# Kernel optimization log

Measured on AMD Instinct MI355X. Metric: run time of the kernel, lower is better.

Reference implementation:

```python
import jax, jax.numpy as jnp
import numpy as np

B, T, H = 64, 320, 256
D = 2 * H  # input_size; cat([cw, cell]) has dim 2*D which must equal 4*H


def setup_inputs() -> dict:
    key = jax.random.key(0)
    ks = jax.random.split(key, 10)
    sD = 1.0 / np.sqrt(D)
    sG = 1.0 / np.sqrt(2 * D)
    sH = 1.0 / np.sqrt(H)
    f32 = jnp.float32
    n = lambda k, shape, s: jax.random.normal(k, shape, dtype=f32) * s
    return {
        "v": n(ks[0], (B, T, D), 1.0),
        "W1": n(ks[1], (D, D), sD), "b1": jnp.zeros((D,), f32),
        "W2": n(ks[2], (D, D), sD), "b2": jnp.zeros((D,), f32),
        "Wg": n(ks[3], (2 * D, 2 * D), sG), "bg": jnp.zeros((2 * D,), f32),
        "Wih_f": n(ks[4], (3 * H, 2 * D), sG), "Whh_f": n(ks[5], (3 * H, H), sH),
        "bih_f": jnp.zeros((3 * H,), f32), "bhh_f": jnp.zeros((3 * H,), f32),
        "Wih_b": n(ks[6], (3 * H, 2 * D), sG), "Whh_b": n(ks[7], (3 * H, H), sH),
        "bih_b": jnp.zeros((3 * H,), f32), "bhh_b": jnp.zeros((3 * H,), f32),
    }


def _gru_cell(x, h, Wih, Whh, bih, bhh):
    # torch GRUCell math: gates ordered (r, z, n)
    gi = x @ Wih.T + bih          # (B, 3H)
    gh = h @ Whh.T + bhh          # (B, 3H)
    i_r, i_z, i_n = jnp.split(gi, 3, axis=-1)
    h_r, h_z, h_n = jnp.split(gh, 3, axis=-1)
    r = jax.nn.sigmoid(i_r + h_r)
    z = jax.nn.sigmoid(i_z + h_z)
    n = jnp.tanh(i_n + r * h_n)
    return (1.0 - z) * n + z * h


def reference(v, W1, b1, W2, b2, Wg, bg,
              Wih_f, Whh_f, bih_f, bhh_f,
              Wih_b, Whh_b, bih_b, bhh_b):
    # context_mult = linear2(v) is identical every timestep -> hoist out of loop
    cm = jnp.einsum('btd,ed->bte', v, W2) + b2          # (B, T, D)

    def step(carry, cw):
        hf, hb = carry                                   # (B, H) each
        cwm = cw @ W1.T + b1                             # (B, D)
        f = jnp.tanh(cwm[:, None, :] + cm)               # (B, T, D)
        scores = jnp.einsum('bd,btd->bt', cw, f)         # (B, T)
        attn = jax.nn.softmax(scores, axis=-1)
        cell = jnp.einsum('bt,btd->bd', attn, v)         # (B, D)
        pg = jnp.concatenate([cw, cell], axis=-1)        # (B, 2D) == (B, 4H)
        gate = jax.nn.sigmoid(pg @ Wg.T + bg)
        gi = pg * gate
        # length-1 bidirectional GRU step: each direction sees the same input
        hf2 = _gru_cell(gi, hf, Wih_f, Whh_f, bih_f, bhh_f)
        hb2 = _gru_cell(gi, hb, Wih_b, Whh_b, bih_b, bhh_b)
        return (hf2, hb2), jnp.concatenate([hf2, hb2], axis=-1)

    h0 = jnp.zeros((v.shape[0], H), v.dtype)
    _, hs = jax.lax.scan(step, (h0, h0), jnp.swapaxes(v, 0, 1))
    return hs  # (T, B, 2H)
```

## Files before the change

### kernel.cpp

```cpp
#include <hip/hip_runtime.h>

typedef unsigned short u16;
typedef __fp16 h2 __attribute__((ext_vector_type(2)));
typedef __attribute__((ext_vector_type(8))) short bf16x8;
typedef __attribute__((ext_vector_type(4))) float f32x4;

__device__ __forceinline__ float fast_exp(float x) { return __expf(x); }
__device__ __forceinline__ float fast_rcp(float x) { return __builtin_amdgcn_rcpf(x); }
__device__ __forceinline__ float fast_tanh(float x) {
  float e = fast_exp(2.0f * x);
  return 1.0f - 2.0f * fast_rcp(e + 1.0f);
}
__device__ __forceinline__ float fast_sigmoid(float x) {
  return fast_rcp(1.0f + fast_exp(-x));
}
__device__ __forceinline__ u16 f2bf(float x) {
  unsigned u = __float_as_uint(x);
  return (u16)((u + 0x7fffu + ((u >> 16) & 1u)) >> 16);
}
__device__ __forceinline__ float bf2f(u16 u) {
  return __uint_as_float(((unsigned)u) << 16);
}

__global__ __launch_bounds__(256)
void k_cvt(const float* __restrict__ src, u16* __restrict__ dst, int n4)
{
  int i = blockIdx.x * 256 + threadIdx.x;
  if (i < n4) {
    float4 x = ((const float4*)src)[i];
    ushort4 o;
    o.x = f2bf(x.x); o.y = f2bf(x.y); o.z = f2bf(x.z); o.w = f2bf(x.w);
    ((ushort4*)dst)[i] = o;
  }
}

__global__ __launch_bounds__(256)
void k_split(const float* __restrict__ src, u16* __restrict__ hi,
             u16* __restrict__ lo, int n4)
{
  int i = blockIdx.x * 256 + threadIdx.x;
  if (i < n4) {
    float4 x = ((const float4*)src)[i];
    ushort4 h, l;
    h.x = f2bf(x.x); l.x = f2bf(x.x - bf2f(h.x));
    h.y = f2bf(x.y); l.y = f2bf(x.y - bf2f(h.y));
    h.z = f2bf(x.z); l.z = f2bf(x.z - bf2f(h.z));
    h.w = f2bf(x.w); l.w = f2bf(x.w - bf2f(h.w));
    ((ushort4*)hi)[i] = h;
    ((ushort4*)lo)[i] = l;
  }
}

template<int EXPOUT>
__global__ __launch_bounds__(256)
void k_sgemm(const u16* __restrict__ Ahi, const u16* __restrict__ Alo,
             const u16* __restrict__ Whi, const u16* __restrict__ Wlo,
             const float* __restrict__ bias,
             float* __restrict__ C, int N, int K, int Tc, int t0)
{
  __shared__ alignas(16) u16 Ah[128][40];
  __shared__ alignas(16) u16 Al[128][40];
  __shared__ alignas(16) u16 Bh[128][40];
  __shared__ alignas(16) u16 Bl[128][40];
  const int tid = threadIdx.x;
  const int m0 = blockIdx.x * 128;
  const int n0 = blockIdx.y * 128;
  const int wave = tid >> 6, lane = tid & 63;
  const int wm = (wave & 1) * 64, wn = (wave >> 1) * 64;

  const u16 *pAh[2], *pAl[2], *pBh[2], *pBl[2];
#pragma unroll
  for (int r = 0; r < 2; ++r) {
    int row = r * 64 + (tid >> 2);
    int gm = m0 + row;
    int ar = (gm / Tc) * 320 + t0 + gm % Tc;
    pAh[r] = Ahi + (size_t)ar * K;
    pAl[r] = Alo + (size_t)ar * K;
    int gn = n0 + row;
    pBh[r] = Whi + (size_t)gn * K;
    pBl[r] = Wlo + (size_t)gn * K;
  }

  f32x4 acc[4][4];
#pragma unroll
  for (int a = 0; a < 4; ++a)
#pragma unroll
    for (int b = 0; b < 4; ++b) acc[a][b] = (f32x4){0.f, 0.f, 0.f, 0.f};

  const int lrow = lane & 15, lq = lane >> 4;

  for (int k0 = 0; k0 < K; k0 += 32) {
#pragma unroll
    for (int r = 0; r < 2; ++r) {
      int row = r * 64 + (tid >> 2);
      int kk = k0 + (tid & 3) * 8;
      *(int4*)&Ah[row][(tid & 3) * 8] = *(const int4*)(pAh[r] + kk);
      *(int4*)&Al[row][(tid & 3) * 8] = *(const int4*)(pAl[r] + kk);
      *(int4*)&Bh[row][(tid & 3) * 8] = *(const int4*)(pBh[r] + kk);
      *(int4*)&Bl[row][(tid & 3) * 8] = *(const int4*)(pBl[r] + kk);
    }
    __syncthreads();
    bf16x8 avh[4], avl[4], bvh[4], bvl[4];
#pragma unroll
    for (int f = 0; f < 4; ++f) {
      avh[f] = *(const bf16x8*)&Ah[wm + f * 16 + lrow][lq * 8];
      avl[f] = *(const bf16x8*)&Al[wm + f * 16 + lrow][lq * 8];
      bvh[f] = *(const bf16x8*)&Bh[wn + f * 16 + lrow][lq * 8];
      bvl[f] = *(const bf16x8*)&Bl[wn + f * 16 + lrow][lq * 8];
    }
#pragma unroll
    for (int mf = 0; mf < 4; ++mf)
#pragma unroll
      for (int nf = 0; nf < 4; ++nf) {
        acc[mf][nf] = __builtin_amdgcn_mfma_f32_16x16x32_bf16(
            avh[mf], bvh[nf], acc[mf][nf], 0, 0, 0);
        acc[mf][nf] = __builtin_amdgcn_mfma_f32_16x16x32_bf16(
            avh[mf], bvl[nf], acc[mf][nf], 0, 0, 0);
        acc[mf][nf] = __builtin_amdgcn_mfma_f32_16x16x32_bf16(
            avl[mf], bvh[nf], acc[mf][nf], 0, 0, 0);
      }
    __syncthreads();
  }

  const int c = lane & 15, rg = lane >> 4;
#pragma unroll
  for (int mf = 0; mf < 4; ++mf) {
#pragma unroll
    for (int r = 0; r < 4; ++r) {
      int m = m0 + wm + mf * 16 + rg * 4 + r;
#pragma unroll
      for (int nf = 0; nf < 4; ++nf) {
        int n = n0 + wn + nf * 16 + c;
        float x = acc[mf][nf][r] + bias[n];
        C[(size_t)m * N + n] = EXPOUT ? fast_exp(2.0f * x) : x;
      }
    }
  }
}

template<int MODE>
__global__ __launch_bounds__(256)
void k_mgemm(const u16* __restrict__ A1, int K1, int map1,
             const u16* __restrict__ A2,
             const u16* __restrict__ W16, const float* __restrict__ bias,
             const float* __restrict__ E1, const float* __restrict__ E2,
             void* __restrict__ Cout, int N, int K, int Tc, int t0)
{
  __shared__ alignas(16) u16 As[128][40];
  __shared__ alignas(16) u16 Bs[128][40];
  const int tid = threadIdx.x;
  const int m0 = blockIdx.x * 128;
  const int n0 = blockIdx.y * 128;
  const int wave = tid >> 6, lane = tid & 63;
  const int wm = (wave & 1) * 64, wn = (wave >> 1) * 64;
  const int K2 = K - K1;

  const u16* pA1r[2];
  const u16* pA2r[2];
  const u16* pWr[2];
#pragma unroll
  for (int r = 0; r < 2; ++r) {
    int row = r * 64 + (tid >> 2);
    int gm = m0 + row;
    int ar1 = map1 ? ((gm / Tc) * 320 + t0 + gm % Tc) : gm;
    pA1r[r] = A1 + (size_t)ar1 * K1;
    pA2r[r] = A2 ? (A2 + (size_t)gm * K2) : pA1r[r];
    pWr[r] = W16 + (size_t)(n0 + row) * K;
  }

  f32x4 acc[4][4];
#pragma unroll
  for (int a = 0; a < 4; ++a)
#pragma unroll
    for (int b = 0; b < 4; ++b) acc[a][b] = (f32x4){0.f, 0.f, 0.f, 0.f};

  const int lrow = lane & 15, lq = lane >> 4;

  for (int k0 = 0; k0 < K; k0 += 32) {
#pragma unroll
    for (int r = 0; r < 2; ++r) {
      int row = r * 64 + (tid >> 2);
      int kk = k0 + (tid & 3) * 8;
      const u16* s = (kk < K1) ? (pA1r[r] + kk) : (pA2r[r] + (kk - K1));
      *(int4*)&As[row][(tid & 3) * 8] = *(const int4*)s;
      *(int4*)&Bs[row][(tid & 3) * 8] = *(const int4*)(pWr[r] + kk);
    }
    __syncthreads();
    bf16x8 av[4], bv[4];
#pragma unroll
    for (int f = 0; f < 4; ++f) {
      av[f] = *(const bf16x8*)&As[wm + f * 16 + lrow][lq * 8];
      bv[f] = *(const bf16x8*)&Bs[wn + f * 16 + lrow][lq * 8];
    }
#pragma unroll
    for (int mf = 0; mf < 4; ++mf)
#pragma unroll
      for (int nf = 0; nf < 4; ++nf)
        acc[mf][nf] = __builtin_amdgcn_mfma_f32_16x16x32_bf16(
            av[mf], bv[nf], acc[mf][nf], 0, 0, 0);
    __syncthreads();
  }

  const int c = lane & 15, rg = lane >> 4;
#pragma unroll
  for (int mf = 0; mf < 4; ++mf) {
#pragma unroll
    for (int r = 0; r < 4; ++r) {
      int m = m0 + wm + mf * 16 + rg * 4 + r;
      int vrow = map1 ? ((m / Tc) * 320 + t0 + m % Tc) : m;
#pragma unroll
      for (int nf = 0; nf < 4; ++nf) {
        int n = n0 + wn + nf * 16 + c;
        float x = acc[mf][nf][r] + bias[n];
        if (MODE == 1) {
          float pg = (n < 512) ? E1[(size_t)vrow * 512 + n]
                               : E2[(size_t)m * 512 + (n - 512)];
          ((u16*)Cout)[(size_t)m * N + n] = f2bf(pg * fast_sigmoid(x));
        } else {
          ((float*)Cout)[(size_t)m * N + n] = x;
        }
      }
    }
  }
}

__global__ __launch_bounds__(256)
void k_scores(const float* __restrict__ v, const float* __restrict__ Ecwm,
              const float* __restrict__ Fcm, float* __restrict__ sc,
              int Tc, int t0)
{
  __shared__ float vs[32][68], fs[32][68], cs[32][68];
  const int b = blockIdx.x;
  const int tl0 = blockIdx.y * 32;
  const int s0 = blockIdx.z * 32;
  const int tid = threadIdx.x;
  const int tx = tid & 15, ty = tid >> 4;
  const float* srcV = v    + ((size_t)b * 320 + t0 + tl0) * 512;
  const float* srcF = Ecwm + ((size_t)b * Tc + tl0) * 512;
  const float* srcC = Fcm  + ((size_t)b * 320 + s0) * 512;
  float a00 = 0, a01 = 0, a10 = 0, a11 = 0;
  float vs0 = 0, vs1 = 0;
  for (int d0 = 0; d0 < 512; d0 += 64) {
#pragma unroll
    for (int r = 0; r < 2; ++r) {
      int f = r * 256 + tid;
      int row = f >> 4, qq = f & 15;
      *(float4*)&vs[row][qq * 4] = *(const float4*)(srcV + (size_t)row * 512 + d0 + qq * 4);
      *(float4*)&fs[row][qq * 4] = *(const float4*)(srcF + (size_t)row * 512 + d0 + qq * 4);
      *(float4*)&cs[row][qq * 4] = *(const float4*)(srcC + (size_t)row * 512 + d0 + qq * 4);
    }
    __syncthreads();
#pragma unroll 4
    for (int d = 0; d < 64; ++d) {
      float c0 = cs[tx][d], c1 = cs[tx + 16][d];
      float e0 = fs[ty][d], e1 = fs[ty + 16][d];
      float v0 = vs[ty][d], v1 = vs[ty + 16][d];
      vs0 += v0; vs1 += v1;
      a00 = fmaf(v0, fast_rcp(fmaf(e0, c0, 1.0f)), a00);
      a01 = fmaf(v0, fast_rcp(fmaf(e0, c1, 1.0f)), a01);
      a10 = fmaf(v1, fast_rcp(fmaf(e1, c0, 1.0f)), a10);
      a11 = fmaf(v1, fast_rcp(fmaf(e1, c1, 1.0f)), a11);
    }
    __syncthreads();
  }
  float* o = sc + (size_t)b * Tc * 320;
  o[(size_t)(tl0 + ty) * 320 + s0 + tx]           = vs0 - 2.0f * a00;
  o[(size_t)(tl0 + ty) * 320 + s0 + tx + 16]      = vs0 - 2.0f * a01;
  o[(size_t)(tl0 + ty + 16) * 320 + s0 + tx]      = vs1 - 2.0f * a10;
  o[(size_t)(tl0 + ty + 16) * 320 + s0 + tx + 16] = vs1 - 2.0f * a11;
}

__global__ __launch_bounds__(256)
void k_softmax(float* __restrict__ sc)
{
  int wave = threadIdx.x >> 6;
  int lane = threadIdx.x & 63;
  int row = blockIdx.x * 4 + wave;
  float* p = sc + (size_t)row * 320;
  float x[5];
  float mx = -1e30f;
#pragma unroll
  for (int j = 0; j < 5; ++j) { x[j] = p[lane + 64 * j]; mx = fmaxf(mx, x[j]); }
#pragma unroll
  for (int off = 32; off > 0; off >>= 1) mx = fmaxf(mx, __shfl_xor(mx, off));
  float s = 0.f;
#pragma unroll
  for (int j = 0; j < 5; ++j) { x[j] = fast_exp(x[j] - mx); s += x[j]; }
#pragma unroll
  for (int off = 32; off > 0; off >>= 1) s += __shfl_xor(s, off);
  float rinv = fast_rcp(s);
#pragma unroll
  for (int j = 0; j < 5; ++j) p[lane + 64 * j] = x[j] * rinv;
}

__global__ __launch_bounds__(256)
void k_cell(const float* __restrict__ attn, const float* __restrict__ v,
            float* __restrict__ cell, u16* __restrict__ cell16, int Tc)
{
  __shared__ float As[16][32], Bs[16][64];
  const int b = blockIdx.x;
  const int m0 = blockIdx.y * 32;
  const int n0 = blockIdx.z * 64;
  const int tid = threadIdx.x;
  const float* A = attn + (size_t)b * Tc * 320;
  const float* B = v + (size_t)b * 320 * 512;
  float acc[2][4];
#pragma unroll
  for (int i = 0; i < 2; ++i)
#pragma unroll
    for (int j = 0; j < 4; ++j) acc[i][j] = 0.f;
  const int tm = (tid & 15) * 2, tn = (tid >> 4) * 4;
  for (int k0 = 0; k0 < 320; k0 += 16) {
    if (tid < 128) {
      int row = tid >> 2, q = tid & 3;
      float4 x = *(const float4*)(A + (size_t)(m0 + row) * 320 + k0 + q * 4);
      As[q * 4 + 0][row] = x.x;
      As[q * 4 + 1][row] = x.y;
      As[q * 4 + 2][row] = x.z;
      As[q * 4 + 3][row] = x.w;
    }
    {
      int krow = tid >> 4, qq = tid & 15;
      *(float4*)&Bs[krow][qq * 4] =
          *(const float4*)(B + (size_t)(k0 + krow) * 512 + n0 + qq * 4);
    }
    __syncthreads();
#pragma unroll
    for (int k = 0; k < 16; ++k) {
      float a0 = As[k][tm], a1 = As[k][tm + 1];
      float bb[4];
      *(float4*)&bb[0] = *(const float4*)&Bs[k][tn];
#pragma unroll
      for (int j = 0; j < 4; ++j) { acc[0][j] += a0 * bb[j]; acc[1][j] += a1 * bb[j]; }
    }
    __syncthreads();
  }
#pragma unroll
  for (int i = 0; i < 2; ++i) {
    size_t off = ((size_t)b * Tc + m0 + tm + i) * 512 + n0 + tn;
    float4 o = make_float4(acc[i][0], acc[i][1], acc[i][2], acc[i][3]);
    *(float4*)(cell + off) = o;
    ushort4 o16;
    o16.x = f2bf(o.x); o16.y = f2bf(o.y); o16.z = f2bf(o.z); o16.w = f2bf(o.w);
    *(ushort4*)(cell16 + off) = o16;
  }
}

__global__ __launch_bounds__(512)
void k_recur(const float* __restrict__ GIf, const float* __restrict__ GIb,
             const float* __restrict__ Whh_f, const float* __restrict__ Whh_b,
             const float* __restrict__ bhh_f, const float* __restrict__ bhh_b,
             float* __restrict__ out, float* __restrict__ hstate,
             int Tc, int t0, int init)
{
  const int b = blockIdx.x >> 1;
  const int dir = blockIdx.x & 1;
  const int tid = threadIdx.x;
  const int i = tid & 255;
  const int half = __builtin_amdgcn_readfirstlane(tid >> 8);
  const int lane = tid & 63;

  __shared__ float part[3][256];
  __shared__ alignas(8) __fp16 hh16[256];

  const float* Wh  = dir ? Whh_b : Whh_f;
  const float* bhh = dir ? bhh_b : bhh_f;
  const float* GI  = (dir ? GIb : GIf) + (size_t)b * Tc * 768;

  h2 wr[64], wz[64], wn[64];
  {
    const float* Wr = Wh + (size_t)i * 256 + half * 128;
    const float* Wz = Wh + (size_t)(256 + i) * 256 + half * 128;
    const float* Wn = Wh + (size_t)(512 + i) * 256 + half * 128;
#pragma unroll
    for (int qd = 0; qd < 32; ++qd) {
      float4 x = *(const float4*)(Wr + 4 * qd);
      wr[2 * qd]     = __builtin_amdgcn_cvt_pkrtz(x.x, x.y);
      wr[2 * qd + 1] = __builtin_amdgcn_cvt_pkrtz(x.z, x.w);
      float4 y = *(const float4*)(Wz + 4 * qd);
      wz[2 * qd]     = __builtin_amdgcn_cvt_pkrtz(y.x, y.y);
      wz[2 * qd + 1] = __builtin_amdgcn_cvt_pkrtz(y.z, y.w);
      float4 zv = *(const float4*)(Wn + 4 * qd);
      wn[2 * qd]     = __builtin_amdgcn_cvt_pkrtz(zv.x, zv.y);
      wn[2 * qd + 1] = __builtin_amdgcn_cvt_pkrtz(zv.z, zv.w);
    }
  }

  float br = 0.f, bz = 0.f, bn = 0.f, hown = 0.f;
  if (half == 0) {
    br = bhh[i]; bz = bhh[256 + i]; bn = bhh[512 + i];
    hown = init ? 0.f : hstate[(size_t)blockIdx.x * 256 + i];
    hh16[i] = (__fp16)hown;
  }
  float* op = out + (size_t)t0 * 32768 + (size_t)b * 512 + dir * 256 + i;
  __syncthreads();

  int2 hp = *(const int2*)((const char*)hh16 + 8 * lane);

  for (int t = 0; t < Tc; ++t) {
    const float* gi = GI + (size_t)t * 768;
    float gr = 0.f, gz = 0.f, gn = 0.f;
    if (half == 0) { gr = gi[i]; gz = gi[256 + i]; gn = gi[512 + i]; }

    float ar0 = 0.f, az0 = 0.f, an0 = 0.f;
    float ar1 = 0.f, az1 = 0.f, an1 = 0.f;
    const int lbase = half * 32;
#pragma unroll
    for (int p = 0; p < 64; p += 2) {
      h2 h0 = __builtin_bit_cast(h2, __builtin_amdgcn_readlane(hp.x, lbase + (p >> 1)));
      h2 h1 = __builtin_bit_cast(h2, __builtin_amdgcn_readlane(hp.y, lbase + (p >> 1)));
      ar0 = __builtin_amdgcn_fdot2(wr[p], h0, ar0, false);
      az0 = __builtin_amdgcn_fdot2(wz[p], h0, az0, false);
      an0 = __builtin_amdgcn_fdot2(wn[p], h0, an0, false);
      ar1 = __builtin_amdgcn_fdot2(wr[p + 1], h1, ar1, false);
      az1 = __builtin_amdgcn_fdot2(wz[p + 1], h1, az1, false);
      an1 = __builtin_amdgcn_fdot2(wn[p + 1], h1, an1, false);
    }
    float ar = ar0 + ar1, az = az0 + az1, an = an0 + an1;
    if (half == 1) {
      part[0][i] = ar; part[1][i] = az; part[2][i] = an;
    }
    __syncthreads();
    if (half == 0) {
      float r  = fast_sigmoid(gr + ar + part[0][i] + br);
      float z  = fast_sigmoid(gz + az + part[1][i] + bz);
      float nn = fast_tanh(gn + r * (an + part[2][i] + bn));
      hown = (1.f - z) * nn + z * hown;
      op[(size_t)t * 32768] = hown;
      hh16[i] = (__fp16)hown;
    }
    __syncthreads();
    hp = *(const int2*)((const char*)hh16 + 8 * lane);
  }
  if (half == 0) hstate[(size_t)blockIdx.x * 256 + i] = hown;
}

extern "C" void kernel_launch(void* const* d_in, const int* in_sizes, int n_in,
                              void* d_out, int out_size, void* d_ws, size_t ws_size,
                              hipStream_t stream)
{
  const float* v     = (const float*)d_in[0];
  const float* W1    = (const float*)d_in[1];
  const float* b1    = (const float*)d_in[2];
  const float* W2    = (const float*)d_in[3];
  const float* b2    = (const float*)d_in[4];
  const float* Wg    = (const float*)d_in[5];
  const float* bg    = (const float*)d_in[6];
  const float* Wih_f = (const float*)d_in[7];
  const float* Whh_f = (const float*)d_in[8];
  const float* bih_f = (const float*)d_in[9];
  const float* bhh_f = (const float*)d_in[10];
  const float* Wih_b = (const float*)d_in[11];
  const float* Whh_b = (const float*)d_in[12];
  const float* bih_b = (const float*)d_in[13];
  const float* bhh_b = (const float*)d_in[14];
  float* out = (float*)d_out;
  float* w = (float*)d_ws;

  int Tc = 32;
  {
    const int cand[4] = {320, 160, 64, 32};
    for (int ci = 0; ci < 4; ++ci) {
      size_t need = 4ull * (22839296ull + 233472ull * (size_t)cand[ci]);
      if (need <= ws_size) { Tc = cand[ci]; break; }
    }
  }
  const int nc = 320 / Tc;

  float* cm     = w;
  float* hstate = w + 10485760;
  u16*  vhi     = (u16*)(w + 10518528);
  u16*  vlo     = (u16*)(w + 15761408);
  u16*  Wg16    = (u16*)(w + 21004288);
  u16*  Wif16   = (u16*)(w + 21528576);
  u16*  Wib16   = (u16*)(w + 21921792);
  u16*  W1hi    = (u16*)(w + 22315008);
  u16*  W1lo    = (u16*)(w + 22446080);
  u16*  W2hi    = (u16*)(w + 22577152);
  u16*  W2lo    = (u16*)(w + 22708224);
  {
    size_t base = 22839296;
    float* cwm;  float* attn;  float* cell;  u16* cell16;  u16* gi16;
    cwm    = w + base;                                  base += (size_t)32768 * Tc;
    attn   = w + base;                                  base += (size_t)20480 * Tc;
    cell   = w + base;                                  base += (size_t)32768 * Tc;
    cell16 = (u16*)(w + base);                          base += (size_t)16384 * Tc;
    gi16   = (u16*)(w + base);                          base += (size_t)32768 * Tc;
    float* GIf = w + base;                              base += (size_t)49152 * Tc;
    float* GIb = w + base;

    k_split<<<(2621440 + 255) / 256, 256, 0, stream>>>(v, vhi, vlo, 2621440);
    k_split<<<(65536 + 255) / 256, 256, 0, stream>>>(W1, W1hi, W1lo, 65536);
    k_split<<<(65536 + 255) / 256, 256, 0, stream>>>(W2, W2hi, W2lo, 65536);
    k_cvt<<<(262144 + 255) / 256, 256, 0, stream>>>(Wg, Wg16, 262144);
    k_cvt<<<(196608 + 255) / 256, 256, 0, stream>>>(Wih_f, Wif16, 196608);
    k_cvt<<<(196608 + 255) / 256, 256, 0, stream>>>(Wih_b, Wib16, 196608);

    k_sgemm<1><<<dim3(160, 4), 256, 0, stream>>>(vhi, vlo, W2hi, W2lo, b2,
                                                 cm, 512, 512, 320, 0);

    for (int c = 0; c < nc; ++c) {
      const int t0 = c * Tc;
      const int Mc = 64 * Tc;
      k_sgemm<1><<<dim3(Mc / 128, 4), 256, 0, stream>>>(vhi, vlo, W1hi, W1lo, b1,
                                                        cwm, 512, 512, Tc, t0);
      k_scores<<<dim3(64, Tc / 32, 10), 256, 0, stream>>>(v, cwm, cm, attn, Tc, t0);
      k_softmax<<<Mc / 4, 256, 0, stream>>>(attn);
      k_cell<<<dim3(64, Tc / 32, 8), 256, 0, stream>>>(attn, v, cell, cell16, Tc);
      k_mgemm<1><<<dim3(Mc / 128, 8), 256, 0, stream>>>(vhi, 512, 1, cell16, Wg16, bg,
                                                        v, cell, gi16, 1024, 1024, Tc, t0);
      k_mgemm<0><<<dim3(Mc / 128, 6), 256, 0, stream>>>(gi16, 1024, 0, nullptr, Wif16, bih_f,
                                                        nullptr, nullptr, GIf, 768, 1024, Tc, t0);
      k_mgemm<0><<<dim3(Mc / 128, 6), 256, 0, stream>>>(gi16, 1024, 0, nullptr, Wib16, bih_b,
                                                        nullptr, nullptr, GIb, 768, 1024, Tc, t0);
      k_recur<<<128, 512, 0, stream>>>(GIf, GIb, Whh_f, Whh_b, bhh_f, bhh_b,
                                       out, hstate, Tc, t0, (c == 0) ? 1 : 0);
    }
  }
}
```

Baseline: 1.564 ms.

## Use direct global-to-LDS loads in GEMMs and split GRU recurrence four ways

The bf16 GEMM kernels now fill their tiles with global_load_lds, which writes straight into LDS without staging through registers, so the tiles become unpadded 32-wide rows. The recurrent GRU kernel is restructured to 1024 threads: each hidden unit's dot product is split across four lanes and reduced with shuffles. It reads the hidden state from a double-buffered LDS array, which drops one barrier per timestep and the readlane broadcasts. The risks are LDS bank conflicts from the unpadded tiles, and higher register pressure and lower occupancy from the 1024-thread launch bound.

```diff
diff --git a/kernel.cpp b/kernel.cpp
--- a/kernel.cpp
+++ b/kernel.cpp
@@ -20,6 +20,11 @@
 }
 __device__ __forceinline__ float bf2f(u16 u) {
   return __uint_as_float(((unsigned)u) << 16);
+}
+__device__ __forceinline__ void gload16(const u16* g, u16* l) {
+  __builtin_amdgcn_global_load_lds(
+      (const __attribute__((address_space(1))) unsigned int*)g,
+      (__attribute__((address_space(3))) unsigned int*)l, 16, 0, 0);
 }
 
 __global__ __launch_bounds__(256)
@@ -58,10 +63,10 @@
              const float* __restrict__ bias,
              float* __restrict__ C, int N, int K, int Tc, int t0)
 {
-  __shared__ alignas(16) u16 Ah[128][40];
-  __shared__ alignas(16) u16 Al[128][40];
-  __shared__ alignas(16) u16 Bh[128][40];
-  __shared__ alignas(16) u16 Bl[128][40];
+  __shared__ alignas(16) u16 Ah[128][32];
+  __shared__ alignas(16) u16 Al[128][32];
+  __shared__ alignas(16) u16 Bh[128][32];
+  __shared__ alignas(16) u16 Bl[128][32];
   const int tid = threadIdx.x;
   const int m0 = blockIdx.x * 128;
   const int n0 = blockIdx.y * 128;
@@ -90,14 +95,13 @@
   const int lrow = lane & 15, lq = lane >> 4;
 
   for (int k0 = 0; k0 < K; k0 += 32) {
+    const int kk = k0 + (tid & 3) * 8;
 #pragma unroll
     for (int r = 0; r < 2; ++r) {
-      int row = r * 64 + (tid >> 2);
-      int kk = k0 + (tid & 3) * 8;
-      *(int4*)&Ah[row][(tid & 3) * 8] = *(const int4*)(pAh[r] + kk);
-      *(int4*)&Al[row][(tid & 3) * 8] = *(const int4*)(pAl[r] + kk);
-      *(int4*)&Bh[row][(tid & 3) * 8] = *(const int4*)(pBh[r] + kk);
-      *(int4*)&Bl[row][(tid & 3) * 8] = *(const int4*)(pBl[r] + kk);
+      gload16(pAh[r] + kk, &Ah[0][0] + r * 2048 + tid * 8);
+      gload16(pAl[r] + kk, &Al[0][0] + r * 2048 + tid * 8);
+      gload16(pBh[r] + kk, &Bh[0][0] + r * 2048 + tid * 8);
+      gload16(pBl[r] + kk, &Bl[0][0] + r * 2048 + tid * 8);
     }
     __syncthreads();
     bf16x8 avh[4], avl[4], bvh[4], bvl[4];
@@ -146,8 +150,8 @@
              const float* __restrict__ E1, const float* __restrict__ E2,
              void* __restrict__ Cout, int N, int K, int Tc, int t0)
 {
-  __shared__ alignas(16) u16 As[128][40];
-  __shared__ alignas(16) u16 Bs[128][40];
+  __shared__ alignas(16) u16 As[128][32];
+  __shared__ alignas(16) u16 Bs[128][32];
   const int tid = threadIdx.x;
   const int m0 = blockIdx.x * 128;
   const int n0 = blockIdx.y * 128;
@@ -177,13 +181,12 @@
   const int lrow = lane & 15, lq = lane >> 4;
 
   for (int k0 = 0; k0 < K; k0 += 32) {
+    const int kk = k0 + (tid & 3) * 8;
 #pragma unroll
     for (int r = 0; r < 2; ++r) {
-      int row = r * 64 + (tid >> 2);
-      int kk = k0 + (tid & 3) * 8;
       const u16* s = (kk < K1) ? (pA1r[r] + kk) : (pA2r[r] + (kk - K1));
-      *(int4*)&As[row][(tid & 3) * 8] = *(const int4*)s;
-      *(int4*)&Bs[row][(tid & 3) * 8] = *(const int4*)(pWr[r] + kk);
+      gload16(s, &As[0][0] + r * 2048 + tid * 8);
+      gload16(pWr[r] + kk, &Bs[0][0] + r * 2048 + tid * 8);
     }
     __syncthreads();
     bf16x8 av[4], bv[4];
@@ -346,7 +349,7 @@
   }
 }
 
-__global__ __launch_bounds__(512)
+__global__ __launch_bounds__(1024)
 void k_recur(const float* __restrict__ GIf, const float* __restrict__ GIb,
              const float* __restrict__ Whh_f, const float* __restrict__ Whh_b,
              const float* __restrict__ bhh_f, const float* __restrict__ bhh_b,
@@ -356,24 +359,23 @@
   const int b = blockIdx.x >> 1;
   const int dir = blockIdx.x & 1;
   const int tid = threadIdx.x;
-  const int i = tid & 255;
-  const int half = __builtin_amdgcn_readfirstlane(tid >> 8);
-  const int lane = tid & 63;
-
-  __shared__ float part[3][256];
-  __shared__ alignas(8) __fp16 hh16[256];
+  const int i = tid >> 2;
+  const int kq = tid & 3;
+  const bool head = (kq == 0);
+
+  __shared__ alignas(16) __fp16 hbuf[2][256];
 
   const float* Wh  = dir ? Whh_b : Whh_f;
   const float* bhh = dir ? bhh_b : bhh_f;
   const float* GI  = (dir ? GIb : GIf) + (size_t)b * Tc * 768;
 
-  h2 wr[64], wz[64], wn[64];
+  h2 wr[32], wz[32], wn[32];
   {
-    const float* Wr = Wh + (size_t)i * 256 + half * 128;
-    const float* Wz = Wh + (size_t)(256 + i) * 256 + half * 128;
-    const float* Wn = Wh + (size_t)(512 + i) * 256 + half * 128;
-#pragma unroll
-    for (int qd = 0; qd < 32; ++qd) {
+    const float* Wr = Wh + (size_t)i * 256 + kq * 64;
+    const float* Wz = Wh + (size_t)(256 + i) * 256 + kq * 64;
+    const float* Wn = Wh + (size_t)(512 + i) * 256 + kq * 64;
+#pragma unroll
+    for (int qd = 0; qd < 16; ++qd) {
       float4 x = *(const float4*)(Wr + 4 * qd);
       wr[2 * qd]     = __builtin_amdgcn_cvt_pkrtz(x.x, x.y);
       wr[2 * qd + 1] = __builtin_amdgcn_cvt_pkrtz(x.z, x.w);
@@ -387,52 +389,57 @@
   }
 
   float br = 0.f, bz = 0.f, bn = 0.f, hown = 0.f;
-  if (half == 0) {
+  if (head) {
     br = bhh[i]; bz = bhh[256 + i]; bn = bhh[512 + i];
     hown = init ? 0.f : hstate[(size_t)blockIdx.x * 256 + i];
-    hh16[i] = (__fp16)hown;
+    hbuf[0][i] = (__fp16)hown;
   }
   float* op = out + (size_t)t0 * 32768 + (size_t)b * 512 + dir * 256 + i;
   __syncthreads();
 
-  int2 hp = *(const int2*)((const char*)hh16 + 8 * lane);
-
   for (int t = 0; t < Tc; ++t) {
+    const int cur = t & 1;
     const float* gi = GI + (size_t)t * 768;
     float gr = 0.f, gz = 0.f, gn = 0.f;
-    if (half == 0) { gr = gi[i]; gz = gi[256 + i]; gn = gi[512 + i]; }
-
-    float ar0 = 0.f, az0 = 0.f, an0 = 0.f;
-    float ar1 = 0.f, az1 = 0.f, an1 = 0.f;
-    const int lbase = half * 32;
-#pragma unroll
-    for (int p = 0; p < 64; p += 2) {
-      h2 h0 = __builtin_bit_cast(h2, __builtin_amdgcn_readlane(hp.x, lbase + (p >> 1)));
-      h2 h1 = __builtin_bit_cast(h2, __builtin_amdgcn_readlane(hp.y, lbase + (p >> 1)));
-      ar0 = __builtin_amdgcn_fdot2(wr[p], h0, ar0, false);
-      az0 = __builtin_amdgcn_fdot2(wz[p], h0, az0, false);
-      an0 = __builtin_amdgcn_fdot2(wn[p], h0, an0, false);
-      ar1 = __builtin_amdgcn_fdot2(wr[p + 1], h1, ar1, false);
-      az1 = __builtin_amdgcn_fdot2(wz[p + 1], h1, az1, false);
-      an1 = __builtin_amdgcn_fdot2(wn[p + 1], h1, an1, false);
-    }
-    float ar = ar0 + ar1, az = az0 + az1, an = an0 + an1;
-    if (half == 1) {
-      part[0][i] = ar; part[1][i] = az; part[2][i] = an;
-    }
-    __syncthreads();
-    if (half == 0) {
-      float r  = fast_sigmoid(gr + ar + part[0][i] + br);
-      float z  = fast_sigmoid(gz + az + part[1][i] + bz);
-      float nn = fast_tanh(gn + r * (an + part[2][i] + bn));
+    if (head) { gr = gi[i]; gz = gi[256 + i]; gn = gi[512 + i]; }
+
+    float ar = 0.f, az = 0.f, an = 0.f;
+    const int4* hp = (const int4*)(&hbuf[cur][kq * 64]);
+#pragma unroll
+    for (int j = 0; j < 8; ++j) {
+      int4 hv = hp[j];
+      h2 h0 = __builtin_bit_cast(h2, hv.x);
+      h2 h1 = __builtin_bit_cast(h2, hv.y);
+      h2 h2v = __builtin_bit_cast(h2, hv.z);
+      h2 h3 = __builtin_bit_cast(h2, hv.w);
+      ar = __builtin_amdgcn_fdot2(wr[4 * j + 0], h0, ar, false);
+      az = __builtin_amdgcn_fdot2(wz[4 * j + 0], h0, az, false);
+      an = __builtin_amdgcn_fdot2(wn[4 * j + 0], h0, an, false);
+      ar = __builtin_amdgcn_fdot2(wr[4 * j + 1], h1, ar, false);
+      az = __builtin_amdgcn_fdot2(wz[4 * j + 1], h1, az, false);
+      an = __builtin_amdgcn_fdot2(wn[4 * j + 1], h1, an, false);
+      ar = __builtin_amdgcn_fdot2(wr[4 * j + 2], h2v, ar, false);
+      az = __builtin_amdgcn_fdot2(wz[4 * j + 2], h2v, az, false);
+      an = __builtin_amdgcn_fdot2(wn[4 * j + 2], h2v, an, false);
+      ar = __builtin_amdgcn_fdot2(wr[4 * j + 3], h3, ar, false);
+      az = __builtin_amdgcn_fdot2(wz[4 * j + 3], h3, az, false);
+      an = __builtin_amdgcn_fdot2(wn[4 * j + 3], h3, an, false);
+    }
+    ar += __shfl_xor(ar, 1); ar += __shfl_xor(ar, 2);
+    az += __shfl_xor(az, 1); az += __shfl_xor(az, 2);
+    an += __shfl_xor(an, 1); an += __shfl_xor(an, 2);
+
+    if (head) {
+      float r  = fast_sigmoid(gr + ar + br);
+      float z  = fast_sigmoid(gz + az + bz);
+      float nn = fast_tanh(gn + r * (an + bn));
       hown = (1.f - z) * nn + z * hown;
       op[(size_t)t * 32768] = hown;
-      hh16[i] = (__fp16)hown;
-    }
-    __syncthreads();
-    hp = *(const int2*)((const char*)hh16 + 8 * lane);
-  }
-  if (half == 0) hstate[(size_t)blockIdx.x * 256 + i] = hown;
+      hbuf[cur ^ 1][i] = (__fp16)hown;
+    }
+    __syncthreads();
+  }
+  if (head) hstate[(size_t)blockIdx.x * 256 + i] = hown;
 }
 
 extern "C" void kernel_launch(void* const* d_in, const int* in_sizes, int n_in,
@@ -513,8 +520,8 @@
                                                         nullptr, nullptr, GIf, 768, 1024, Tc, t0);
       k_mgemm<0><<<dim3(Mc / 128, 6), 256, 0, stream>>>(gi16, 1024, 0, nullptr, Wib16, bih_b,
                                                         nullptr, nullptr, GIb, 768, 1024, Tc, t0);
-      k_recur<<<128, 512, 0, stream>>>(GIf, GIb, Whh_f, Whh_b, bhh_f, bhh_b,
-                                       out, hstate, Tc, t0, (c == 0) ? 1 : 0);
-    }
-  }
-}
+      k_recur<<<128, 1024, 0, stream>>>(GIf, GIb, Whh_f, Whh_b, bhh_f, bhh_b,
+                                        out, hstate, Tc, t0, (c == 0) ? 1 : 0);
+    }
+  }
+}
```

Measured after the change: 1.474 ms. -5.7%, faster.
